# Kernel tuning notes

Hardware: AMD Instinct MI355X
Metric: run time of the kernel (lower is better)

The kernel has to match this reference:

```python
import jax, jax.numpy as jnp
import numpy as np

N_NODES = 100000
N_EDGES = 1600000
N_GRAPHS = 128
IN_CH, OUT_CH, N_CLASS = 768, 128, 2


def setup_inputs() -> dict:
    key = jax.random.key(0)
    ks = jax.random.split(key, 8)
    x = jax.random.normal(ks[0], (N_NODES, IN_CH), dtype=jnp.float32)
    # directed edges with src < dst so to_undirected (concat + reverse) has no duplicates
    src = jax.random.randint(ks[1], (N_EDGES,), 0, N_NODES - 1, dtype=jnp.int32)
    dst = jax.random.randint(ks[2], (N_EDGES,), 1, N_NODES, dtype=jnp.int32)
    dst = jnp.where(dst <= src, src + 1, dst)  # ensure src < dst (no self-loops)
    edge_index = jnp.stack([src, dst], axis=0)
    batch = jnp.sort(jax.random.randint(ks[3], (N_NODES,), 0, N_GRAPHS, dtype=jnp.int32))
    s = 0.05
    return {
        "x": x,
        "edge_index": edge_index,
        "batch": batch,
        "num_graphs": N_GRAPHS,
        "W_conv": jax.random.normal(ks[4], (IN_CH, OUT_CH), dtype=jnp.float32) * s,
        "b_conv": jnp.zeros((OUT_CH,), dtype=jnp.float32),
        "W_lin0": jax.random.normal(ks[5], (IN_CH, OUT_CH), dtype=jnp.float32) * s,
        "b_lin0": jnp.zeros((OUT_CH,), dtype=jnp.float32),
        "W_lin1": jax.random.normal(ks[6], (2 * OUT_CH, OUT_CH), dtype=jnp.float32) * s,
        "b_lin1": jnp.zeros((OUT_CH,), dtype=jnp.float32),
        "W_lin2": jax.random.normal(ks[7], (OUT_CH, N_CLASS), dtype=jnp.float32) * s,
        "b_lin2": jnp.zeros((N_CLASS,), dtype=jnp.float32),
    }


def _gcn_conv(x, W, b, src, dst, n_nodes):
    # GCNConv: linear transform, add self-loops, symmetric normalization, scatter-add
    loop = jnp.arange(n_nodes, dtype=src.dtype)
    s = jnp.concatenate([src, loop])
    d = jnp.concatenate([dst, loop])
    deg = jax.ops.segment_sum(jnp.ones_like(d, dtype=x.dtype), d, num_segments=n_nodes)
    dinv = jnp.where(deg > 0, jax.lax.rsqrt(deg), 0.0)
    norm = dinv[s] * dinv[d]  # [E']
    h = x @ W  # [N, out]
    msg = h[s] * norm[:, None]  # gather + scale
    return jax.ops.segment_sum(msg, d, num_segments=n_nodes) + b


def reference(x, edge_index, batch, num_graphs, W_conv, b_conv,
              W_lin0, b_lin0, W_lin1, b_lin1, W_lin2, b_lin2):
    n_nodes = x.shape[0]
    # to_undirected: add reversed edges (input has src<dst so no duplicates to coalesce)
    src = jnp.concatenate([edge_index[0], edge_index[1]])
    dst = jnp.concatenate([edge_index[1], edge_index[0]])
    h = jax.nn.relu(_gcn_conv(x, W_conv, b_conv, src, dst, n_nodes))
    # global max pool over graphs
    h = jax.ops.segment_max(h, batch, num_segments=num_graphs)  # [G, out]
    # root node = first node of each graph (batch is sorted)
    root = jax.ops.segment_min(jnp.arange(n_nodes), batch, num_segments=num_graphs)
    news = jax.nn.relu(x[root] @ W_lin0 + b_lin0)  # [G, out]
    h = jax.nn.relu(jnp.concatenate([news, h], axis=-1) @ W_lin1 + b_lin1)
    logits = h @ W_lin2 + b_lin2
    return jax.nn.log_softmax(logits, axis=-1)
```

## Files before the change

### kernel.cpp

```cpp
#include <hip/hip_runtime.h>

#define N_NODES 100000
#define N_EDGES 1600000
#define N_GRAPHS 128
#define IN_CH 768
#define OUT_CH 128

#define BSHIFT 8
#define NBKT ((N_NODES + 255) / 256)
#define EPB 4000
#define CAPREC 16384
#define PADV 16
#define CAPADJ (CAPREC + 256 * (PADV - 1))

using short8 = __attribute__((ext_vector_type(8))) short;
using f32x4  = __attribute__((ext_vector_type(4))) float;

__device__ __forceinline__ float bf2f(unsigned short u) {
    return __uint_as_float(((unsigned)u) << 16);
}
__device__ __forceinline__ unsigned short f2bf(float f) {
    unsigned u = __float_as_uint(f);
    u += 0x7fffu + ((u >> 16) & 1u);
    return (unsigned short)(u >> 16);
}
__device__ __forceinline__ float load_f(const void* p, size_t i, int f32) {
    return f32 ? ((const float*)p)[i] : bf2f(((const unsigned short*)p)[i]);
}
__device__ __forceinline__ float lo16(unsigned p) { return __uint_as_float(p << 16); }
__device__ __forceinline__ float hi16(unsigned p) { return __uint_as_float(p & 0xffff0000u); }

__global__ void k_detect(const unsigned short* __restrict__ x, int* flag) {
    __shared__ int s;
    if (threadIdx.x == 0) s = 0;
    __syncthreads();
    int bad = 0;
    for (int j = threadIdx.x; j < 8192; j += 256) {
        float v = bf2f(x[j]);
        if (!(v > -64.f && v < 64.f)) bad = 1;
    }
    if (bad) atomicOr(&s, 1);
    __syncthreads();
    if (threadIdx.x == 0) *flag = s;
}

__global__ void k_init(const int* __restrict__ flag, int* gcur, unsigned* pooled, int* root,
                       const int* __restrict__ batch,
                       const void* Wc, const void* bc, const void* W0, const void* b0,
                       const void* W1, const void* b1, const void* W2, const void* b2,
                       unsigned short* Wt, float* fbc, float* fW0, float* fb0,
                       float* fW1, float* fb1, float* fW2, float* fb2) {
    int f32 = *flag;
    int i = blockIdx.x * blockDim.x + threadIdx.x;
    if (i < NBKT) gcur[i] = i * CAPREC;
    if (i < N_GRAPHS * OUT_CH) pooled[i] = 0u;
    if (i < N_NODES) {
        int b = batch[i];
        if (i == 0 || batch[i - 1] != b) root[b] = i;
    }
    if (i < IN_CH * OUT_CH) {
        int n = i / IN_CH, k = i - n * IN_CH;
        Wt[i] = f32 ? f2bf(((const float*)Wc)[k * OUT_CH + n])
                    : ((const unsigned short*)Wc)[k * OUT_CH + n];
        fW0[i] = load_f(W0, i, f32);
    }
    if (i < 2 * OUT_CH * OUT_CH) fW1[i] = load_f(W1, i, f32);
    if (i < OUT_CH * 2) fW2[i] = load_f(W2, i, f32);
    if (i < OUT_CH) { fbc[i] = load_f(bc, i, f32); fb0[i] = load_f(b0, i, f32); fb1[i] = load_f(b1, i, f32); }
    if (i < 2) fb2[i] = load_f(b2, i, f32);
}

__global__ __launch_bounds__(256) void k_bin(const int* __restrict__ src, const int* __restrict__ dst,
                                             int* gcur, unsigned* __restrict__ binned) {
    __shared__ int hist[NBKT];
    __shared__ int basep[NBKT];
    int t = threadIdx.x;
    for (int b = t; b < NBKT; b += 256) hist[b] = 0;
    __syncthreads();
    int e0 = blockIdx.x * EPB, e1 = e0 + EPB;
    if (e1 > N_EDGES) e1 = N_EDGES;
    for (int i = e0 + t; i < e1; i += 256) {
        unsigned s_ = (unsigned)src[i]; if (s_ >= N_NODES) s_ = N_NODES - 1u;
        unsigned d_ = (unsigned)dst[i]; if (d_ >= N_NODES) d_ = N_NODES - 1u;
        atomicAdd(&hist[d_ >> BSHIFT], 1);
        atomicAdd(&hist[s_ >> BSHIFT], 1);
    }
    __syncthreads();
    for (int b = t; b < NBKT; b += 256) {
        int c = hist[b];
        if (c) {
            int base = atomicAdd(&gcur[b], c);
            basep[b] = (base + c <= (b + 1) * CAPREC) ? base : -1;
        }
        hist[b] = 0;
    }
    __syncthreads();
    for (int i = e0 + t; i < e1; i += 256) {
        unsigned s_ = (unsigned)src[i]; if (s_ >= N_NODES) s_ = N_NODES - 1u;
        unsigned d_ = (unsigned)dst[i]; if (d_ >= N_NODES) d_ = N_NODES - 1u;
        unsigned bd = d_ >> BSHIFT, bs = s_ >> BSHIFT;
        int pd_ = basep[bd], ps_ = basep[bs];
        int od = atomicAdd(&hist[bd], 1);
        int os = atomicAdd(&hist[bs], 1);
        if (pd_ >= 0) binned[pd_ + od] = (s_ << 8) | (d_ & 255u);
        if (ps_ >= 0) binned[ps_ + os] = (d_ << 8) | (s_ & 255u);
    }
}

__global__ __launch_bounds__(256) void k_build(const unsigned* __restrict__ binned,
                                               const int* __restrict__ gcur,
                                               int2* odeg, float* dinv, int* adj) {
    __shared__ int sdeg[256], scur[256], sscan[256];
    int b = blockIdx.x, t = threadIdx.x;
    int base = b * CAPREC;
    int n = gcur[b] - base;
    if (n > CAPREC) n = CAPREC;
    if (n < 0) n = 0;
    int base_adj = b * CAPADJ;
    sdeg[t] = 0;
    __syncthreads();
    for (int j = t; j < n; j += 256) atomicAdd(&sdeg[binned[base + j] & 255u], 1);
    __syncthreads();
    int myd = sdeg[t];
    int pd = (myd + PADV - 1) & ~(PADV - 1);
    sscan[t] = pd;
    __syncthreads();
    for (int off = 1; off < 256; off <<= 1) {
        int add = (t >= off) ? sscan[t - off] : 0;
        __syncthreads();
        sscan[t] += add;
        __syncthreads();
    }
    int excl = sscan[t] - pd;
    int node = (b << BSHIFT) + t;
    if (node < N_NODES) {
        odeg[node] = make_int2(base_adj + excl, pd);
        dinv[node] = rsqrtf((float)(myd + 1));
    }
    for (int j = myd; j < pd; j++) adj[base_adj + excl + j] = N_NODES;
    scur[t] = excl;
    __syncthreads();
    for (int j = t; j < n; j += 256) {
        unsigned rec = binned[base + j];
        int loc = rec & 255u;
        adj[base_adj + atomicAdd(&scur[loc], 1)] = (int)(rec >> 8);
    }
}

#define MBLK 128
#define BK 64
#define LSTR 72

__global__ __launch_bounds__(256) void k_gemm(const int* __restrict__ flag,
                                              const void* __restrict__ xv,
                                              const unsigned short* __restrict__ Wt,
                                              const float* __restrict__ dinv,
                                              unsigned short* __restrict__ h) {
    __shared__ __align__(16) unsigned short As[MBLK * LSTR];
    __shared__ __align__(16) unsigned short Bs[OUT_CH * LSTR];
    const int f32 = *flag;
    const int tid = threadIdx.x;
    if (blockIdx.x == 0 && tid < 64) ((unsigned*)(h + (size_t)N_NODES * OUT_CH))[tid] = 0u;
    const int wave = tid >> 6, lane = tid & 63;
    const int quad = lane >> 4, l16 = lane & 15;
    const int wm = (wave >> 1) * 64, wn = (wave & 1) * 64;
    const int row0 = blockIdx.x * MBLK;

    f32x4 acc[4][4];
#pragma unroll
    for (int mt = 0; mt < 4; mt++)
#pragma unroll
        for (int nt = 0; nt < 4; nt++) acc[mt][nt] = (f32x4){0.f, 0.f, 0.f, 0.f};

    for (int k0 = 0; k0 < IN_CH; k0 += BK) {
#pragma unroll
        for (int i = 0; i < 4; i++) {
            int chunk = tid + i * 256;
            int r = chunk >> 3, c8 = (chunk & 7) << 3;
            int gr = row0 + r; if (gr >= N_NODES) gr = N_NODES - 1;
            uint4 va;
            if (f32) {
                const float* xp = (const float*)xv + (size_t)gr * IN_CH + k0 + c8;
                float4 f0 = *(const float4*)xp;
                float4 f1 = *(const float4*)(xp + 4);
                va.x = (unsigned)f2bf(f0.x) | ((unsigned)f2bf(f0.y) << 16);
                va.y = (unsigned)f2bf(f0.z) | ((unsigned)f2bf(f0.w) << 16);
                va.z = (unsigned)f2bf(f1.x) | ((unsigned)f2bf(f1.y) << 16);
                va.w = (unsigned)f2bf(f1.z) | ((unsigned)f2bf(f1.w) << 16);
            } else {
                va = *(const uint4*)((const unsigned short*)xv + (size_t)gr * IN_CH + k0 + c8);
            }
            *(uint4*)&As[r * LSTR + c8] = va;
            uint4 vb = *(const uint4*)(Wt + (size_t)r * IN_CH + k0 + c8);
            *(uint4*)&Bs[r * LSTR + c8] = vb;
        }
        __syncthreads();
#pragma unroll
        for (int kk = 0; kk < BK; kk += 32) {
            short8 af[4], bf[4];
#pragma unroll
            for (int mt = 0; mt < 4; mt++)
                af[mt] = *(const short8*)&As[(wm + mt * 16 + l16) * LSTR + kk + quad * 8];
#pragma unroll
            for (int nt = 0; nt < 4; nt++)
                bf[nt] = *(const short8*)&Bs[(wn + nt * 16 + l16) * LSTR + kk + quad * 8];
#pragma unroll
            for (int mt = 0; mt < 4; mt++)
#pragma unroll
                for (int nt = 0; nt < 4; nt++)
                    acc[mt][nt] = __builtin_amdgcn_mfma_f32_16x16x32_bf16(af[mt], bf[nt], acc[mt][nt], 0, 0, 0);
        }
        __syncthreads();
    }

#pragma unroll
    for (int mt = 0; mt < 4; mt++) {
#pragma unroll
        for (int r = 0; r < 4; r++) {
            int m = row0 + wm + mt * 16 + quad * 4 + r;
            if (m >= N_NODES) continue;
            float dvm = dinv[m];
#pragma unroll
            for (int nt = 0; nt < 4; nt++) {
                int col = wn + nt * 16 + l16;
                h[(size_t)m * OUT_CH + col] = f2bf(acc[mt][nt][r] * dvm);
            }
        }
    }
}

__global__ __launch_bounds__(256) void k_agg(const unsigned short* __restrict__ h,
                                             const int* __restrict__ adj,
                                             const int2* __restrict__ odeg,
                                             const float* __restrict__ dinv,
                                             const int* __restrict__ batch,
                                             const float* __restrict__ fbc,
                                             unsigned* pooled) {
    int wave = threadIdx.x >> 6, lane = threadIdx.x & 63;
    int node = blockIdx.x * 4 + wave;
    float dv = dinv[node];

    unsigned hv = *(const unsigned*)(h + (size_t)node * OUT_CH + lane * 2);
    float a0 = lo16(hv);
    float a1 = hi16(hv);

    int2 od = odeg[node];
    int o = od.x, e = od.x + od.y;
    for (int i = o; i < e; i += 16) {
        uint4 q0 = *(const uint4*)&adj[i];
        uint4 q1 = *(const uint4*)&adj[i + 4];
        uint4 q2 = *(const uint4*)&adj[i + 8];
        uint4 q3 = *(const uint4*)&adj[i + 12];
        unsigned p0 = *(const unsigned*)(h + (size_t)q0.x * OUT_CH + lane * 2);
        unsigned p1 = *(const unsigned*)(h + (size_t)q0.y * OUT_CH + lane * 2);
        unsigned p2 = *(const unsigned*)(h + (size_t)q0.z * OUT_CH + lane * 2);
        unsigned p3 = *(const unsigned*)(h + (size_t)q0.w * OUT_CH + lane * 2);
        unsigned p4 = *(const unsigned*)(h + (size_t)q1.x * OUT_CH + lane * 2);
        unsigned p5 = *(const unsigned*)(h + (size_t)q1.y * OUT_CH + lane * 2);
        unsigned p6 = *(const unsigned*)(h + (size_t)q1.z * OUT_CH + lane * 2);
        unsigned p7 = *(const unsigned*)(h + (size_t)q1.w * OUT_CH + lane * 2);
        unsigned p8 = *(const unsigned*)(h + (size_t)q2.x * OUT_CH + lane * 2);
        unsigned p9 = *(const unsigned*)(h + (size_t)q2.y * OUT_CH + lane * 2);
        unsigned pa = *(const unsigned*)(h + (size_t)q2.z * OUT_CH + lane * 2);
        unsigned pb = *(const unsigned*)(h + (size_t)q2.w * OUT_CH + lane * 2);
        unsigned pc = *(const unsigned*)(h + (size_t)q3.x * OUT_CH + lane * 2);
        unsigned pd = *(const unsigned*)(h + (size_t)q3.y * OUT_CH + lane * 2);
        unsigned pe = *(const unsigned*)(h + (size_t)q3.z * OUT_CH + lane * 2);
        unsigned pf = *(const unsigned*)(h + (size_t)q3.w * OUT_CH + lane * 2);
        a0 += (((lo16(p0) + lo16(p1)) + (lo16(p2) + lo16(p3)))
             + ((lo16(p4) + lo16(p5)) + (lo16(p6) + lo16(p7))))
            + (((lo16(p8) + lo16(p9)) + (lo16(pa) + lo16(pb)))
             + ((lo16(pc) + lo16(pd)) + (lo16(pe) + lo16(pf))));
        a1 += (((hi16(p0) + hi16(p1)) + (hi16(p2) + hi16(p3)))
             + ((hi16(p4) + hi16(p5)) + (hi16(p6) + hi16(p7))))
            + (((hi16(p8) + hi16(p9)) + (hi16(pa) + hi16(pb)))
             + ((hi16(pc) + hi16(pd)) + (hi16(pe) + hi16(pf))));
    }
    a0 = fmaxf(fmaf(a0, dv, fbc[lane * 2]), 0.f);
    a1 = fmaxf(fmaf(a1, dv, fbc[lane * 2 + 1]), 0.f);

    int g = batch[node];
    __shared__ float s0[256], s1[256];
    __shared__ int sg[4];
    s0[threadIdx.x] = a0; s1[threadIdx.x] = a1;
    if (lane == 0) sg[wave] = g;
    __syncthreads();
    if (wave == 0) {
        int g0 = sg[0];
        if (sg[1] == g0 && sg[2] == g0 && sg[3] == g0) {
            float m0 = fmaxf(fmaxf(s0[lane], s0[64 + lane]), fmaxf(s0[128 + lane], s0[192 + lane]));
            float m1 = fmaxf(fmaxf(s1[lane], s1[64 + lane]), fmaxf(s1[128 + lane], s1[192 + lane]));
            atomicMax(&pooled[g0 * OUT_CH + lane * 2],     __float_as_uint(m0));
            atomicMax(&pooled[g0 * OUT_CH + lane * 2 + 1], __float_as_uint(m1));
        } else {
#pragma unroll
            for (int w = 0; w < 4; w++) {
                atomicMax(&pooled[sg[w] * OUT_CH + lane * 2],     __float_as_uint(s0[w * 64 + lane]));
                atomicMax(&pooled[sg[w] * OUT_CH + lane * 2 + 1], __float_as_uint(s1[w * 64 + lane]));
            }
        }
    }
}

__global__ __launch_bounds__(256) void k_final(const int* __restrict__ flag,
                                               const void* __restrict__ x,
                                               const int* __restrict__ root,
                                               const unsigned* __restrict__ pooled,
                                               const float* __restrict__ W0,
                                               const float* __restrict__ b0,
                                               const float* __restrict__ W1,
                                               const float* __restrict__ b1,
                                               const float* __restrict__ W2,
                                               const float* __restrict__ b2,
                                               void* out) {
    __shared__ float xs[IN_CH];
    __shared__ float ps[256];
    __shared__ float ins[2 * OUT_CH];
    __shared__ float h2s[OUT_CH];
    int f32 = *flag;
    int g = blockIdx.x, t = threadIdx.x;
    int r = root[g]; if ((unsigned)r >= N_NODES) r = 0;
    for (int j = t; j < IN_CH; j += 256) xs[j] = load_f(x, (size_t)r * IN_CH + j, f32);
    if (t >= 128) ins[OUT_CH + (t - 128)] = __uint_as_float(pooled[g * OUT_CH + (t - 128)]);
    __syncthreads();
    {
        int c = t & 127, half = t >> 7;
        int k0 = half * (IN_CH / 2);
        float acc = 0.f;
#pragma unroll 8
        for (int k = 0; k < IN_CH / 2; k++) acc += xs[k0 + k] * W0[(size_t)(k0 + k) * OUT_CH + c];
        ps[t] = acc;
    }
    __syncthreads();
    if (t < 128) ins[t] = fmaxf(ps[t] + ps[t + 128] + b0[t], 0.f);
    __syncthreads();
    {
        int c = t & 127, half = t >> 7;
        int k0 = half * OUT_CH;
        float acc = 0.f;
#pragma unroll 8
        for (int k = 0; k < OUT_CH; k++) acc += ins[k0 + k] * W1[(size_t)(k0 + k) * OUT_CH + c];
        ps[t] = acc;
    }
    __syncthreads();
    if (t < 128) h2s[t] = fmaxf(ps[t] + ps[t + 128] + b1[t], 0.f);
    __syncthreads();
    if (t == 0) {
        float l0 = b2[0], l1 = b2[1];
        for (int k = 0; k < OUT_CH; k++) { float v = h2s[k]; l0 += v * W2[k * 2]; l1 += v * W2[k * 2 + 1]; }
        float m = fmaxf(l0, l1);
        float ls = m + logf(expf(l0 - m) + expf(l1 - m));
        if (f32) {
            ((float*)out)[g * 2]     = l0 - ls;
            ((float*)out)[g * 2 + 1] = l1 - ls;
        } else {
            ((unsigned short*)out)[g * 2]     = f2bf(l0 - ls);
            ((unsigned short*)out)[g * 2 + 1] = f2bf(l1 - ls);
        }
    }
}

extern "C" void kernel_launch(void* const* d_in, const int* in_sizes, int n_in,
                              void* d_out, int out_size, void* d_ws, size_t ws_size,
                              hipStream_t stream) {
    const void* x     = d_in[0];
    const int*  ei    = (const int*)d_in[1];
    const int*  batch = (const int*)d_in[2];
    const void* Wc    = d_in[4];
    const void* bc    = d_in[5];
    const void* W0    = d_in[6];
    const void* b0    = d_in[7];
    const void* W1    = d_in[8];
    const void* b1    = d_in[9];
    const void* W2    = d_in[10];
    const void* b2    = d_in[11];
    const int* src = ei;
    const int* dst = ei + N_EDGES;

    char* p = (char*)d_ws;
    auto carve = [&](size_t bytes) -> void* {
        void* r = (void*)p;
        p += (bytes + 255) & ~(size_t)255;
        return r;
    };
    int*      flag      = (int*)carve(4);
    int*      gcur      = (int*)carve((size_t)NBKT * 4);
    int2*     odeg      = (int2*)carve((size_t)N_NODES * 8);
    float*    dinv      = (float*)carve((size_t)N_NODES * 4);
    int*      root      = (int*)carve(128 * 4);
    unsigned* pooled    = (unsigned*)carve((size_t)N_GRAPHS * OUT_CH * 4);
    unsigned short* Wt  = (unsigned short*)carve((size_t)IN_CH * OUT_CH * 2);
    float*    fW0       = (float*)carve((size_t)IN_CH * OUT_CH * 4);
    float*    fW1       = (float*)carve((size_t)2 * OUT_CH * OUT_CH * 4);
    float*    fW2       = (float*)carve((size_t)OUT_CH * 2 * 4);
    float*    fbc       = (float*)carve((size_t)OUT_CH * 4);
    float*    fb0       = (float*)carve((size_t)OUT_CH * 4);
    float*    fb1       = (float*)carve((size_t)OUT_CH * 4);
    float*    fb2       = (float*)carve(2 * 4);
    int*      adj       = (int*)carve((size_t)NBKT * CAPADJ * 4);
    size_t binned_bytes = (size_t)NBKT * CAPREC * 4;
    size_t h_bytes      = (size_t)(N_NODES + 1) * OUT_CH * 2;
    void*     hb        = carve(binned_bytes > h_bytes ? binned_bytes : h_bytes);
    unsigned* binned    = (unsigned*)hb;
    unsigned short* h   = (unsigned short*)hb;

    const int nEdgeBlk = (N_EDGES + EPB - 1) / EPB;

    k_detect<<<1, 256, 0, stream>>>((const unsigned short*)x, flag);
    k_init  <<<391, 256, 0, stream>>>(flag, gcur, pooled, root, batch, Wc, bc, W0, b0, W1, b1, W2, b2,
                                      Wt, fbc, fW0, fb0, fW1, fb1, fW2, fb2);
    k_bin   <<<nEdgeBlk, 256, 0, stream>>>(src, dst, gcur, binned);
    k_build <<<NBKT, 256, 0, stream>>>(binned, gcur, odeg, dinv, adj);
    k_gemm  <<<(N_NODES + MBLK - 1) / MBLK, 256, 0, stream>>>(flag, x, Wt, dinv, h);
    k_agg   <<<N_NODES / 4, 256, 0, stream>>>(h, adj, odeg, dinv, batch, fbc, pooled);
    k_final <<<N_GRAPHS, 256, 0, stream>>>(flag, x, root, pooled, fW0, fb0, fW1, fb1, fW2, fb2, d_out);
}
```

Before: 708.5 us.

## Widen aggregation gathers, prefetch GEMM tiles, merge detect into init

The aggregation kernel now has each wave load four neighbour rows per instruction with 16-byte loads, 16 lanes per row and 8 channels per lane, then sums the four partial results with xor shuffles. This replaces sixteen separate 4-byte loads per iteration and is meant to cut memory instruction count and latency in the gather-bound stage. The GEMM main loop prefetches the next K tile into registers while MFMAs run on the current shared tile, to overlap global loads with compute at the cost of extra registers. The input dtype detection moves into k_init, which removes one kernel launch but makes every init block repeat the 8192-element scan, and edges per bin block are doubled.

```diff
diff --git a/kernel.cpp b/kernel.cpp
--- a/kernel.cpp
+++ b/kernel.cpp
@@ -8,7 +8,7 @@
 
 #define BSHIFT 8
 #define NBKT ((N_NODES + 255) / 256)
-#define EPB 4000
+#define EPB 8000
 #define CAPREC 16384
 #define PADV 16
 #define CAPADJ (CAPREC + 256 * (PADV - 1))
@@ -30,28 +30,25 @@
 __device__ __forceinline__ float lo16(unsigned p) { return __uint_as_float(p << 16); }
 __device__ __forceinline__ float hi16(unsigned p) { return __uint_as_float(p & 0xffff0000u); }
 
-__global__ void k_detect(const unsigned short* __restrict__ x, int* flag) {
-    __shared__ int s;
-    if (threadIdx.x == 0) s = 0;
-    __syncthreads();
-    int bad = 0;
-    for (int j = threadIdx.x; j < 8192; j += 256) {
-        float v = bf2f(x[j]);
-        if (!(v > -64.f && v < 64.f)) bad = 1;
-    }
-    if (bad) atomicOr(&s, 1);
-    __syncthreads();
-    if (threadIdx.x == 0) *flag = s;
-}
-
-__global__ void k_init(const int* __restrict__ flag, int* gcur, unsigned* pooled, int* root,
-                       const int* __restrict__ batch,
+__global__ void k_init(int* flag, int* gcur, unsigned* pooled, int* root,
+                       const int* __restrict__ batch, const unsigned short* __restrict__ xbits,
                        const void* Wc, const void* bc, const void* W0, const void* b0,
                        const void* W1, const void* b1, const void* W2, const void* b2,
                        unsigned short* Wt, float* fbc, float* fW0, float* fb0,
                        float* fW1, float* fb1, float* fW2, float* fb2) {
-    int f32 = *flag;
+    __shared__ int sflag;
+    if (threadIdx.x == 0) sflag = 0;
+    __syncthreads();
+    int bad = 0;
+    for (int j = threadIdx.x; j < 8192; j += 256) {
+        float v = bf2f(xbits[j]);
+        if (!(v > -64.f && v < 64.f)) bad = 1;
+    }
+    if (bad) atomicOr(&sflag, 1);
+    __syncthreads();
+    int f32 = sflag;
     int i = blockIdx.x * blockDim.x + threadIdx.x;
+    if (i == 0) *flag = f32;
     if (i < NBKT) gcur[i] = i * CAPREC;
     if (i < N_GRAPHS * OUT_CH) pooled[i] = 0u;
     if (i < N_NODES) {
@@ -172,44 +169,81 @@
 #pragma unroll
         for (int nt = 0; nt < 4; nt++) acc[mt][nt] = (f32x4){0.f, 0.f, 0.f, 0.f};
 
-    for (int k0 = 0; k0 < IN_CH; k0 += BK) {
-#pragma unroll
-        for (int i = 0; i < 4; i++) {
-            int chunk = tid + i * 256;
-            int r = chunk >> 3, c8 = (chunk & 7) << 3;
-            int gr = row0 + r; if (gr >= N_NODES) gr = N_NODES - 1;
-            uint4 va;
-            if (f32) {
-                const float* xp = (const float*)xv + (size_t)gr * IN_CH + k0 + c8;
-                float4 f0 = *(const float4*)xp;
-                float4 f1 = *(const float4*)(xp + 4);
-                va.x = (unsigned)f2bf(f0.x) | ((unsigned)f2bf(f0.y) << 16);
-                va.y = (unsigned)f2bf(f0.z) | ((unsigned)f2bf(f0.w) << 16);
-                va.z = (unsigned)f2bf(f1.x) | ((unsigned)f2bf(f1.y) << 16);
-                va.w = (unsigned)f2bf(f1.z) | ((unsigned)f2bf(f1.w) << 16);
-            } else {
-                va = *(const uint4*)((const unsigned short*)xv + (size_t)gr * IN_CH + k0 + c8);
-            }
-            *(uint4*)&As[r * LSTR + c8] = va;
-            uint4 vb = *(const uint4*)(Wt + (size_t)r * IN_CH + k0 + c8);
-            *(uint4*)&Bs[r * LSTR + c8] = vb;
-        }
+    int r_[4], c8_[4];
+    size_t arow_[4];
+#pragma unroll
+    for (int i = 0; i < 4; i++) {
+        int chunk = tid + i * 256;
+        r_[i] = chunk >> 3;
+        c8_[i] = (chunk & 7) << 3;
+        int gr = row0 + r_[i]; if (gr >= N_NODES) gr = N_NODES - 1;
+        arow_[i] = (size_t)gr * IN_CH;
+    }
+
+    float4 fa[4][2];
+    uint4  ua[4];
+    uint4  rb[4];
+
+#define LOADK(K0)                                                                      \
+    {                                                                                  \
+        if (f32) {                                                                     \
+            _Pragma("unroll") for (int i = 0; i < 4; i++) {                            \
+                const float* xp = (const float*)xv + arow_[i] + (K0) + c8_[i];         \
+                fa[i][0] = *(const float4*)xp;                                         \
+                fa[i][1] = *(const float4*)(xp + 4);                                   \
+            }                                                                          \
+        } else {                                                                       \
+            _Pragma("unroll") for (int i = 0; i < 4; i++)                              \
+                ua[i] = *(const uint4*)((const unsigned short*)xv + arow_[i] + (K0) + c8_[i]); \
+        }                                                                              \
+        _Pragma("unroll") for (int i = 0; i < 4; i++)                                  \
+            rb[i] = *(const uint4*)(Wt + (size_t)r_[i] * IN_CH + (K0) + c8_[i]);       \
+    }
+
+#define STOREK()                                                                       \
+    {                                                                                  \
+        if (f32) {                                                                     \
+            _Pragma("unroll") for (int i = 0; i < 4; i++) {                            \
+                uint4 va;                                                              \
+                va.x = (unsigned)f2bf(fa[i][0].x) | ((unsigned)f2bf(fa[i][0].y) << 16);\
+                va.y = (unsigned)f2bf(fa[i][0].z) | ((unsigned)f2bf(fa[i][0].w) << 16);\
+                va.z = (unsigned)f2bf(fa[i][1].x) | ((unsigned)f2bf(fa[i][1].y) << 16);\
+                va.w = (unsigned)f2bf(fa[i][1].z) | ((unsigned)f2bf(fa[i][1].w) << 16);\
+                *(uint4*)&As[r_[i] * LSTR + c8_[i]] = va;                              \
+                *(uint4*)&Bs[r_[i] * LSTR + c8_[i]] = rb[i];                           \
+            }                                                                          \
+        } else {                                                                       \
+            _Pragma("unroll") for (int i = 0; i < 4; i++) {                            \
+                *(uint4*)&As[r_[i] * LSTR + c8_[i]] = ua[i];                           \
+                *(uint4*)&Bs[r_[i] * LSTR + c8_[i]] = rb[i];                           \
+            }                                                                          \
+        }                                                                              \
+    }
+
+#define COMPUTE()                                                                      \
+    {                                                                                  \
+        _Pragma("unroll") for (int kk = 0; kk < BK; kk += 32) {                        \
+            short8 af[4], bf[4];                                                       \
+            _Pragma("unroll") for (int mt = 0; mt < 4; mt++)                           \
+                af[mt] = *(const short8*)&As[(wm + mt * 16 + l16) * LSTR + kk + quad * 8]; \
+            _Pragma("unroll") for (int nt = 0; nt < 4; nt++)                           \
+                bf[nt] = *(const short8*)&Bs[(wn + nt * 16 + l16) * LSTR + kk + quad * 8]; \
+            _Pragma("unroll") for (int mt = 0; mt < 4; mt++)                           \
+                _Pragma("unroll") for (int nt = 0; nt < 4; nt++)                       \
+                    acc[mt][nt] = __builtin_amdgcn_mfma_f32_16x16x32_bf16(af[mt], bf[nt], acc[mt][nt], 0, 0, 0); \
+        }                                                                              \
+    }
+
+    LOADK(0);
+    STOREK();
+    __syncthreads();
+    for (int k0 = BK;; k0 += BK) {
+        bool more = (k0 < IN_CH);
+        if (more) LOADK(k0);
+        COMPUTE();
+        if (!more) break;
         __syncthreads();
-#pragma unroll
-        for (int kk = 0; kk < BK; kk += 32) {
-            short8 af[4], bf[4];
-#pragma unroll
-            for (int mt = 0; mt < 4; mt++)
-                af[mt] = *(const short8*)&As[(wm + mt * 16 + l16) * LSTR + kk + quad * 8];
-#pragma unroll
-            for (int nt = 0; nt < 4; nt++)
-                bf[nt] = *(const short8*)&Bs[(wn + nt * 16 + l16) * LSTR + kk + quad * 8];
-#pragma unroll
-            for (int mt = 0; mt < 4; mt++)
-#pragma unroll
-                for (int nt = 0; nt < 4; nt++)
-                    acc[mt][nt] = __builtin_amdgcn_mfma_f32_16x16x32_bf16(af[mt], bf[nt], acc[mt][nt], 0, 0, 0);
-        }
+        STOREK();
         __syncthreads();
     }
 
@@ -227,6 +261,9 @@
             }
         }
     }
+#undef LOADK
+#undef STOREK
+#undef COMPUTE
 }
 
 __global__ __launch_bounds__(256) void k_agg(const unsigned short* __restrict__ h,
@@ -239,51 +276,65 @@
     int wave = threadIdx.x >> 6, lane = threadIdx.x & 63;
     int node = blockIdx.x * 4 + wave;
     float dv = dinv[node];
-
-    unsigned hv = *(const unsigned*)(h + (size_t)node * OUT_CH + lane * 2);
-    float a0 = lo16(hv);
-    float a1 = hi16(hv);
+    int l16 = lane & 15;
+
+    uint4 own = *(const uint4*)(h + (size_t)node * OUT_CH + l16 * 8);
+    float gsel = (lane < 16) ? 1.f : 0.f;
+    float a0 = lo16(own.x) * gsel, a1 = hi16(own.x) * gsel;
+    float a2 = lo16(own.y) * gsel, a3 = hi16(own.y) * gsel;
+    float a4 = lo16(own.z) * gsel, a5 = hi16(own.z) * gsel;
+    float a6 = lo16(own.w) * gsel, a7 = hi16(own.w) * gsel;
 
     int2 od = odeg[node];
     int o = od.x, e = od.x + od.y;
+#define GATH(q)                                                              \
+    {                                                                        \
+        unsigned rlo = (lane & 16) ? (q).y : (q).x;                          \
+        unsigned rhi = (lane & 16) ? (q).w : (q).z;                          \
+        unsigned row = (lane & 32) ? rhi : rlo;                              \
+        uint4 pv = *(const uint4*)(h + (size_t)row * OUT_CH + l16 * 8);      \
+        a0 += lo16(pv.x); a1 += hi16(pv.x);                                  \
+        a2 += lo16(pv.y); a3 += hi16(pv.y);                                  \
+        a4 += lo16(pv.z); a5 += hi16(pv.z);                                  \
+        a6 += lo16(pv.w); a7 += hi16(pv.w);                                  \
+    }
     for (int i = o; i < e; i += 16) {
         uint4 q0 = *(const uint4*)&adj[i];
         uint4 q1 = *(const uint4*)&adj[i + 4];
         uint4 q2 = *(const uint4*)&adj[i + 8];
         uint4 q3 = *(const uint4*)&adj[i + 12];
-        unsigned p0 = *(const unsigned*)(h + (size_t)q0.x * OUT_CH + lane * 2);
-        unsigned p1 = *(const unsigned*)(h + (size_t)q0.y * OUT_CH + lane * 2);
-        unsigned p2 = *(const unsigned*)(h + (size_t)q0.z * OUT_CH + lane * 2);
-        unsigned p3 = *(const unsigned*)(h + (size_t)q0.w * OUT_CH + lane * 2);
-        unsigned p4 = *(const unsigned*)(h + (size_t)q1.x * OUT_CH + lane * 2);
-        unsigned p5 = *(const unsigned*)(h + (size_t)q1.y * OUT_CH + lane * 2);
-        unsigned p6 = *(const unsigned*)(h + (size_t)q1.z * OUT_CH + lane * 2);
-        unsigned p7 = *(const unsigned*)(h + (size_t)q1.w * OUT_CH + lane * 2);
-        unsigned p8 = *(const unsigned*)(h + (size_t)q2.x * OUT_CH + lane * 2);
-        unsigned p9 = *(const unsigned*)(h + (size_t)q2.y * OUT_CH + lane * 2);
-        unsigned pa = *(const unsigned*)(h + (size_t)q2.z * OUT_CH + lane * 2);
-        unsigned pb = *(const unsigned*)(h + (size_t)q2.w * OUT_CH + lane * 2);
-        unsigned pc = *(const unsigned*)(h + (size_t)q3.x * OUT_CH + lane * 2);
-        unsigned pd = *(const unsigned*)(h + (size_t)q3.y * OUT_CH + lane * 2);
-        unsigned pe = *(const unsigned*)(h + (size_t)q3.z * OUT_CH + lane * 2);
-        unsigned pf = *(const unsigned*)(h + (size_t)q3.w * OUT_CH + lane * 2);
-        a0 += (((lo16(p0) + lo16(p1)) + (lo16(p2) + lo16(p3)))
-             + ((lo16(p4) + lo16(p5)) + (lo16(p6) + lo16(p7))))
-            + (((lo16(p8) + lo16(p9)) + (lo16(pa) + lo16(pb)))
-             + ((lo16(pc) + lo16(pd)) + (lo16(pe) + lo16(pf))));
-        a1 += (((hi16(p0) + hi16(p1)) + (hi16(p2) + hi16(p3)))
-             + ((hi16(p4) + hi16(p5)) + (hi16(p6) + hi16(p7))))
-            + (((hi16(p8) + hi16(p9)) + (hi16(pa) + hi16(pb)))
-             + ((hi16(pc) + hi16(pd)) + (hi16(pe) + hi16(pf))));
-    }
-    a0 = fmaxf(fmaf(a0, dv, fbc[lane * 2]), 0.f);
-    a1 = fmaxf(fmaf(a1, dv, fbc[lane * 2 + 1]), 0.f);
+        GATH(q0) GATH(q1) GATH(q2) GATH(q3)
+    }
+#undef GATH
+
+    a0 += __shfl_xor(a0, 16, 64); a1 += __shfl_xor(a1, 16, 64);
+    a2 += __shfl_xor(a2, 16, 64); a3 += __shfl_xor(a3, 16, 64);
+    a4 += __shfl_xor(a4, 16, 64); a5 += __shfl_xor(a5, 16, 64);
+    a6 += __shfl_xor(a6, 16, 64); a7 += __shfl_xor(a7, 16, 64);
+    a0 += __shfl_xor(a0, 32, 64); a1 += __shfl_xor(a1, 32, 64);
+    a2 += __shfl_xor(a2, 32, 64); a3 += __shfl_xor(a3, 32, 64);
+    a4 += __shfl_xor(a4, 32, 64); a5 += __shfl_xor(a5, 32, 64);
+    a6 += __shfl_xor(a6, 32, 64); a7 += __shfl_xor(a7, 32, 64);
+
+    float4 bA = *(const float4*)&fbc[l16 * 8];
+    float4 bB = *(const float4*)&fbc[l16 * 8 + 4];
+    float r0 = fmaxf(fmaf(a0, dv, bA.x), 0.f);
+    float r1 = fmaxf(fmaf(a1, dv, bA.y), 0.f);
+    float r2 = fmaxf(fmaf(a2, dv, bA.z), 0.f);
+    float r3 = fmaxf(fmaf(a3, dv, bA.w), 0.f);
+    float r4 = fmaxf(fmaf(a4, dv, bB.x), 0.f);
+    float r5 = fmaxf(fmaf(a5, dv, bB.y), 0.f);
+    float r6 = fmaxf(fmaf(a6, dv, bB.z), 0.f);
+    float r7 = fmaxf(fmaf(a7, dv, bB.w), 0.f);
 
     int g = batch[node];
     __shared__ float s0[256], s1[256];
     __shared__ int sg[4];
-    s0[threadIdx.x] = a0; s1[threadIdx.x] = a1;
-    if (lane == 0) sg[wave] = g;
+    if (lane < 16) {
+        *(float4*)&s0[wave * 64 + l16 * 4] = (float4){r0, r2, r4, r6};
+        *(float4*)&s1[wave * 64 + l16 * 4] = (float4){r1, r3, r5, r7};
+        if (l16 == 0) sg[wave] = g;
+    }
     __syncthreads();
     if (wave == 0) {
         int g0 = sg[0];
@@ -406,8 +457,8 @@
 
     const int nEdgeBlk = (N_EDGES + EPB - 1) / EPB;
 
-    k_detect<<<1, 256, 0, stream>>>((const unsigned short*)x, flag);
-    k_init  <<<391, 256, 0, stream>>>(flag, gcur, pooled, root, batch, Wc, bc, W0, b0, W1, b1, W2, b2,
+    k_init  <<<391, 256, 0, stream>>>(flag, gcur, pooled, root, batch, (const unsigned short*)x,
+                                      Wc, bc, W0, b0, W1, b1, W2, b2,
                                       Wt, fbc, fW0, fb0, fW1, fb1, fW2, fb2);
     k_bin   <<<nEdgeBlk, 256, 0, stream>>>(src, dst, gcur, binned);
     k_build <<<NBKT, 256, 0, stream>>>(binned, gcur, odeg, dinv, adj);
```

Result: no change. 697.5 us (-1.6%).
